# Kernel tuning notes

Measured on AMD Instinct MI355X. Metric: run time of the kernel, lower is better.

The kernel has to match this reference:

```python
import jax, jax.numpy as jnp
import numpy as np

G = 88        # voxel grid side
N = 200000    # active voxels
C = 64        # channels
P = 65536     # padded pairs per kernel offset
EPS = 1e-5


def _build_sparse_inputs():
    rng = np.random.default_rng(0)
    lin = rng.choice(G ** 3, size=N, replace=False)
    coords = np.stack(np.unravel_index(lin, (G, G, G)), axis=1).astype(np.int64)
    B = G + 2
    key = lambda c: ((c[:, 0] + 1) * B + (c[:, 1] + 1)) * B + (c[:, 2] + 1)
    keys = key(coords)
    order = np.argsort(keys)
    skeys = keys[order]
    offsets = [(i, j, k) for i in (-1, 0, 1) for j in (-1, 0, 1) for k in (-1, 0, 1)
               if (i, j, k) != (0, 0, 0)]
    in_maps = np.full((26, P), N, np.int32)   # sentinel N -> zero row
    out_maps = np.full((26, P), N, np.int32)  # sentinel N -> dump row
    for idx, off in enumerate(offsets):
        tgt = coords + np.array(off)
        tk = key(tgt)
        pos = np.clip(np.searchsorted(skeys, tk), 0, N - 1)
        valid = skeys[pos] == tk
        ii = order[pos[valid]]
        oo = np.nonzero(valid)[0]
        m = min(len(ii), P)
        in_maps[idx, :m] = ii[:m].astype(np.int32)
        out_maps[idx, :m] = oo[:m].astype(np.int32)
    return jnp.asarray(in_maps), jnp.asarray(out_maps)


def setup_inputs() -> dict:
    key = jax.random.key(0)
    ks = jax.random.split(key, 3)
    in_maps, out_maps = _build_sparse_inputs()
    return {
        "x": jax.random.normal(ks[0], (N, C), jnp.float32),
        "W1": jax.random.normal(ks[1], (27, C, C), jnp.float32) * 0.05,
        "gamma1": jnp.ones((C,), jnp.float32),
        "beta1": jnp.zeros((C,), jnp.float32),
        "W2": jax.random.normal(ks[2], (27, C, C), jnp.float32) * 0.05,
        "gamma2": jnp.ones((C,), jnp.float32),
        "beta2": jnp.zeros((C,), jnp.float32),
        "in_maps": in_maps,
        "out_maps": out_maps,
    }


def _sparse_conv3(feats, W, in_maps, out_maps):
    # feats: [N, Cin]; W: [27, Cin, Cout]; maps: [26, P] (center offset = W[13])
    n = feats.shape[0]
    zero_row = jnp.zeros((1, feats.shape[1]), feats.dtype)
    xp = jnp.concatenate([feats, zero_row], axis=0)          # [N+1, Cin]
    out = jnp.pad(feats @ W[13], ((0, 1), (0, 0)))            # center + dump row
    W_off = jnp.concatenate([W[:13], W[14:]], axis=0)         # [26, Cin, Cout]
    gathered = xp[in_maps]                                    # [26, P, Cin]
    contrib = jnp.einsum('kpc,kcd->kpd', gathered, W_off)     # [26, P, Cout]
    out = out.at[out_maps.reshape(-1)].add(contrib.reshape(-1, contrib.shape[-1]))
    return out[:n]


def _batch_norm(h, gamma, beta):
    mu = h.mean(axis=0)
    var = h.var(axis=0)  # biased, matches torch BN normalization
    return gamma * (h - mu) * jax.lax.rsqrt(var + EPS) + beta


def reference(x, W1, gamma1, beta1, W2, gamma2, beta2, in_maps, out_maps):
    out = _sparse_conv3(x, W1, in_maps, out_maps)
    out = jax.nn.relu(_batch_norm(out, gamma1, beta1))
    out = _batch_norm(_sparse_conv3(out, W2, in_maps, out_maps), gamma2, beta2)
    return jax.nn.relu(out + x)
```

## Files before the change

### kernel.cpp

```cpp
#include <hip/hip_runtime.h>
#include <hip/hip_bf16.h>


#define N_VOX 200000
#define NP 200192
#define EPS_BN 1e-5f

typedef __attribute__((ext_vector_type(8))) short bf16x8;
typedef __attribute__((ext_vector_type(4))) float f32x4;


__global__ void fill_kernel(int* __restrict__ nbrT, float* __restrict__ sums) {
    int p = blockIdx.y;
    long i = ((long)blockIdx.x * 256 + threadIdx.x) * 4;
    if (i < NP) {
        int4 v;
        if (p == 13) {
            v.x = (i + 0 < N_VOX) ? (int)i + 0 : N_VOX;
            v.y = (i + 1 < N_VOX) ? (int)i + 1 : N_VOX;
            v.z = (i + 2 < N_VOX) ? (int)i + 2 : N_VOX;
            v.w = (i + 3 < N_VOX) ? (int)i + 3 : N_VOX;
        } else {
            v.x = v.y = v.z = v.w = N_VOX;
        }
        *(int4*)(nbrT + (long)p * NP + i) = v;
    }
    if (p == 0 && blockIdx.x == 0 && threadIdx.x < 64) {
        float4 z = {0.f, 0.f, 0.f, 0.f};
        ((float4*)sums)[threadIdx.x] = z;
    }
}

__global__ void scatter_kernel(const int* __restrict__ out_maps,
                               const int* __restrict__ in_maps,
                               int* __restrict__ nbrT) {
    int idx = blockIdx.x * 256 + threadIdx.x;
    int o = out_maps[idx];
    if (o < N_VOX) {
        int k = idx >> 16;
        int p = k + (k >= 13);
        nbrT[(long)p * NP + o] = in_maps[idx];
    }
}

__global__ void cast_x_kernel(const float* __restrict__ x,
                              __hip_bfloat16* __restrict__ xb) {
    long i = ((long)blockIdx.x * 256 + threadIdx.x) * 4;
    if (i >= (long)(N_VOX + 1) * 64) return;
    __hip_bfloat16 t[4];
    if (i < (long)N_VOX * 64) {
        float4 v = *(const float4*)(x + i);
        t[0] = __float2bfloat16(v.x); t[1] = __float2bfloat16(v.y);
        t[2] = __float2bfloat16(v.z); t[3] = __float2bfloat16(v.w);
    } else {
        t[0] = t[1] = t[2] = t[3] = __float2bfloat16(0.0f);
    }
    *(ushort4*)(xb + i) = *(ushort4*)t;
}

__global__ void cast_w_kernel(const float* __restrict__ W1, const float* __restrict__ W2,
                              __hip_bfloat16* __restrict__ W1S, __hip_bfloat16* __restrict__ W2S) {
    int idx = blockIdx.x * 256 + threadIdx.x;
    if (idx >= 27 * 4096) return;
    int j    = idx & 7;
    int lane = (idx >> 3) & 63;
    int g    = idx >> 9;
    int half = g & 1, ct = (g >> 1) & 3, k = g >> 3;
    int m = lane & 15, quad = lane >> 4;
    int c = half * 32 + quad * 8 + j;
    int d = ct * 16 + m;
    int src = k * 4096 + c * 64 + d;
    W1S[idx] = __float2bfloat16(W1[src]);
    W2S[idx] = __float2bfloat16(W2[src]);
}


__global__ __launch_bounds__(256, 3) void conv_kernel(
    const __hip_bfloat16* __restrict__ xb,
    const __hip_bfloat16* __restrict__ W4,
    const int* __restrict__ nbrT,
    __hip_bfloat16* __restrict__ h,
    float* __restrict__ sums)
{
    const int tid  = threadIdx.x;
    const int lane = tid & 63;
    const int wave = tid >> 6;
    const int m    = lane & 15;
    const int quad = lane >> 4;
    const int blockbase = blockIdx.x * 256;
    const int rbase = blockbase + wave * 64;

    __shared__ __align__(16) char smem[52224];
    int*            sidx = (int*)smem;
    __hip_bfloat16* bbuf = (__hip_bfloat16*)(smem + 27648);
    float*          lsum = (float*)(smem + 44032);
    float*          lsq  = (float*)(smem + 48128);
    __hip_bfloat16* trans = (__hip_bfloat16*)(smem + wave * 9216);

    for (int j = tid; j < 27 * 256; j += 256)
        sidx[j] = nbrT[(long)(j >> 8) * NP + blockbase + (j & 255)];

    {
        const __hip_bfloat16* ws = W4 + wave * 1024 + lane * 8;
        bf16x8 b0 = *(const bf16x8*)(ws);
        bf16x8 b1 = *(const bf16x8*)(ws + 512);
        __hip_bfloat16* bd = bbuf + wave * 1024 + lane * 8;
        *(bf16x8*)bd = b0;
        *(bf16x8*)(bd + 512) = b1;
    }
    __syncthreads();

    f32x4 acc[16];
#pragma unroll
    for (int i = 0; i < 16; ++i) acc[i] = (f32x4){0.f, 0.f, 0.f, 0.f};

    const bf16x8 z8 = {0, 0, 0, 0, 0, 0, 0, 0};
    bf16x8 A[2][4][2];
    bf16x8 btr0, btr1;

#define LOAD_A(s, p)                                                        \
    {                                                                       \
        _Pragma("unroll")                                                   \
        for (int t = 0; t < 4; ++t) {                                       \
            int ii = sidx[(p) * 256 + wave * 64 + t * 16 + m];              \
            if (ii < N_VOX) {                                               \
                const __hip_bfloat16* rr = xb + (long)ii * 64 + quad * 8;   \
                A[s][t][0] = *(const bf16x8*)rr;                            \
                A[s][t][1] = *(const bf16x8*)(rr + 32);                     \
            } else { A[s][t][0] = z8; A[s][t][1] = z8; }                    \
        }                                                                   \
    }

#define LOAD_BT(p)                                                          \
    {                                                                       \
        const __hip_bfloat16* ws = W4 + (p) * 4096 + wave * 1024 + lane * 8;\
        btr0 = *(const bf16x8*)(ws);                                        \
        btr1 = *(const bf16x8*)(ws + 512);                                  \
    }

    LOAD_BT(1)
    LOAD_A(0, 0)

#pragma unroll
    for (int k = 0; k < 27; ++k) {
        asm volatile("s_waitcnt lgkmcnt(0)\n\ts_barrier" ::: "memory");
        if (k + 1 < 27) {
            __hip_bfloat16* bd = bbuf + ((k + 1) & 1) * 4096 + wave * 1024 + lane * 8;
            *(bf16x8*)bd = btr0;
            *(bf16x8*)(bd + 512) = btr1;
        }
        if (k + 2 < 27) LOAD_BT(k + 2)
        if (k + 1 < 27) LOAD_A((k + 1) & 1, k + 1)
        __builtin_amdgcn_sched_barrier(0);
        const __hip_bfloat16* bb = bbuf + (k & 1) * 4096;
        const int cs = k & 1;
#pragma unroll
        for (int ct = 0; ct < 4; ++ct) {
#pragma unroll
            for (int hf = 0; hf < 2; ++hf) {
                bf16x8 b = *(const bf16x8*)(bb + (ct * 2 + hf) * 512 + lane * 8);
#pragma unroll
                for (int t = 0; t < 4; ++t)
                    acc[t * 4 + ct] = __builtin_amdgcn_mfma_f32_16x16x32_bf16(A[cs][t][hf], b, acc[t * 4 + ct], 0, 0, 0);
            }
        }
        __builtin_amdgcn_sched_barrier(0);
    }
#undef LOAD_A
#undef LOAD_BT

    __syncthreads();

    const bool valid = rbase < N_VOX;

#pragma unroll
    for (int ct = 0; ct < 4; ++ct) {
        float s = 0.f, q = 0.f;
        if (valid) {
#pragma unroll
            for (int t = 0; t < 4; ++t)
#pragma unroll
                for (int r = 0; r < 4; ++r) {
                    float v = acc[t * 4 + ct][r];
                    s += v; q += v * v;
                }
        }
        lsum[(wave * 4 + quad) * 64 + ct * 16 + m] = s;
        lsq [(wave * 4 + quad) * 64 + ct * 16 + m] = q;
    }
    __syncthreads();
    if (tid < 64) {
        float S = 0.f, Q = 0.f;
#pragma unroll
        for (int j = 0; j < 16; ++j) { S += lsum[j * 64 + tid]; Q += lsq[j * 64 + tid]; }
        atomicAdd(&sums[tid], S);
        atomicAdd(&sums[64 + tid], Q);
    }

    if (valid) {
#pragma unroll
        for (int t = 0; t < 4; ++t)
#pragma unroll
            for (int r = 0; r < 4; ++r)
#pragma unroll
                for (int ct = 0; ct < 4; ++ct)
                    trans[(t * 16 + quad * 4 + r) * 72 + ct * 16 + m] =
                        __float2bfloat16(acc[t * 4 + ct][r]);
#pragma unroll
        for (int i = 0; i < 8; ++i) {
            int row = i * 8 + (lane >> 3);
            bf16x8 v = *(const bf16x8*)(trans + row * 72 + (lane & 7) * 8);
            *(bf16x8*)(h + (long)(rbase + row) * 64 + (lane & 7) * 8) = v;
        }
    }
}


__global__ void bnrelu_kernel(const __hip_bfloat16* __restrict__ h, const float* __restrict__ sums,
                              const float* __restrict__ gamma, const float* __restrict__ beta,
                              __hip_bfloat16* __restrict__ hb) {
    long i = ((long)blockIdx.x * 256 + threadIdx.x) * 4;
    if (i >= (long)(N_VOX + 1) * 64) return;
    __hip_bfloat16 t[4];
    if (i < (long)N_VOX * 64) {
        int c0 = (int)(i & 63);
        ushort4 raw = *(const ushort4*)(h + i);
        __hip_bfloat16 hv[4];
        *(ushort4*)hv = raw;
#pragma unroll
        for (int j = 0; j < 4; ++j) {
            int c = c0 + j;
            float mu  = sums[c] * (1.0f / N_VOX);
            float var = sums[64 + c] * (1.0f / N_VOX) - mu * mu;
            float rs  = rsqrtf(var + EPS_BN);
            float val = gamma[c] * (__bfloat162float(hv[j]) - mu) * rs + beta[c];
            t[j] = __float2bfloat16(fmaxf(val, 0.0f));
        }
    } else {
        t[0] = t[1] = t[2] = t[3] = __float2bfloat16(0.0f);
    }
    *(ushort4*)(hb + i) = *(ushort4*)t;
}


__global__ void final_kernel(const __hip_bfloat16* __restrict__ h, const float* __restrict__ x,
                             const float* __restrict__ sums, const float* __restrict__ gamma,
                             const float* __restrict__ beta, float* __restrict__ out) {
    long i = ((long)blockIdx.x * 256 + threadIdx.x) * 4;
    if (i >= (long)N_VOX * 64) return;
    int c0 = (int)(i & 63);
    ushort4 raw = *(const ushort4*)(h + i);
    __hip_bfloat16 hv[4];
    *(ushort4*)hv = raw;
    float4 xr = *(const float4*)(x + i);
    float xx[4] = {xr.x, xr.y, xr.z, xr.w};
    float oo[4];
#pragma unroll
    for (int j = 0; j < 4; ++j) {
        int c = c0 + j;
        float mu  = sums[c] * (1.0f / N_VOX);
        float var = sums[64 + c] * (1.0f / N_VOX) - mu * mu;
        float rs  = rsqrtf(var + EPS_BN);
        float val = gamma[c] * (__bfloat162float(hv[j]) - mu) * rs + beta[c] + xx[j];
        oo[j] = fmaxf(val, 0.0f);
    }
    float4 ov = {oo[0], oo[1], oo[2], oo[3]};
    *(float4*)(out + i) = ov;
}


extern "C" void kernel_launch(void* const* d_in, const int* in_sizes, int n_in,
                              void* d_out, int out_size, void* d_ws, size_t ws_size,
                              hipStream_t stream) {
    const float* x      = (const float*)d_in[0];
    const float* W1     = (const float*)d_in[1];
    const float* gamma1 = (const float*)d_in[2];
    const float* beta1  = (const float*)d_in[3];
    const float* W2     = (const float*)d_in[4];
    const float* gamma2 = (const float*)d_in[5];
    const float* beta2  = (const float*)d_in[6];
    const int* in_maps  = (const int*)d_in[7];
    const int* out_maps = (const int*)d_in[8];
    float* out = (float*)d_out;

    char* ws = (char*)d_ws;
    size_t off = 0;
    auto alloc = [&](size_t bytes) -> void* {
        void* p = ws + off;
        off = (off + bytes + 255) & ~(size_t)255;
        return p;
    };
    int* nbrT           = (int*)alloc((size_t)27 * NP * 4);
    __hip_bfloat16* xb  = (__hip_bfloat16*)alloc((size_t)(N_VOX + 1) * 64 * 2);
    __hip_bfloat16* W1S = (__hip_bfloat16*)alloc((size_t)27 * 4096 * 2);
    __hip_bfloat16* W2S = (__hip_bfloat16*)alloc((size_t)27 * 4096 * 2);
    __hip_bfloat16* h   = (__hip_bfloat16*)alloc((size_t)N_VOX * 64 * 2);
    float* sums         = (float*)alloc(256 * 4);
    __hip_bfloat16* h1b = xb;

    const long elem_x = (long)(N_VOX + 1) * 64;

    fill_kernel   <<<dim3((NP / 4 + 255) / 256, 27), 256, 0, stream>>>(nbrT, sums);
    scatter_kernel<<<26 * 65536 / 256, 256, 0, stream>>>(out_maps, in_maps, nbrT);
    cast_x_kernel <<<(int)((elem_x / 4 + 255) / 256), 256, 0, stream>>>(x, xb);
    cast_w_kernel <<<(27 * 4096 + 255) / 256, 256, 0, stream>>>(W1, W2, W1S, W2S);

    conv_kernel   <<<NP / 256, 256, 0, stream>>>(xb, W1S, nbrT, h, sums);
    bnrelu_kernel <<<(int)((elem_x / 4 + 255) / 256), 256, 0, stream>>>(h, sums, gamma1, beta1, h1b);

    conv_kernel   <<<NP / 256, 256, 0, stream>>>(h1b, W2S, nbrT, h, sums + 128);
    final_kernel  <<<(int)(((long)N_VOX * 64 / 4 + 255) / 256), 256, 0, stream>>>(h, x, sums + 128, gamma2, beta2, out);
}
```

Baseline: 340.5 us.

## Vectorize neighbor index loads, reduce BN stats via wave shuffles, template sentinel check

The 27x256 neighbor-index tile is now loaded as int4 vectors instead of scalar ints. Per-block BN statistics are reduced with cross-quad wave shuffles and direct per-wave atomics, which removes the LDS lsum/lsq buffers and one barrier and cuts shared memory so more blocks may fit. A DIAG template parameter drops the sentinel branch for the first conv. That relies on xb holding a zeroed extra row at index N_VOX, while the second conv keeps the check. Atomic traffic to the sums array rises fourfold in exchange.

```diff
diff --git a/kernel.cpp b/kernel.cpp
--- a/kernel.cpp
+++ b/kernel.cpp
@@ -75,6 +75,7 @@
 }
 
 
+template<int DIAG>
 __global__ __launch_bounds__(256, 3) void conv_kernel(
     const __hip_bfloat16* __restrict__ xb,
     const __hip_bfloat16* __restrict__ W4,
@@ -90,15 +91,15 @@
     const int blockbase = blockIdx.x * 256;
     const int rbase = blockbase + wave * 64;
 
-    __shared__ __align__(16) char smem[52224];
+    __shared__ __align__(16) char smem[44032];
     int*            sidx = (int*)smem;
     __hip_bfloat16* bbuf = (__hip_bfloat16*)(smem + 27648);
-    float*          lsum = (float*)(smem + 44032);
-    float*          lsq  = (float*)(smem + 48128);
     __hip_bfloat16* trans = (__hip_bfloat16*)(smem + wave * 9216);
 
-    for (int j = tid; j < 27 * 256; j += 256)
-        sidx[j] = nbrT[(long)(j >> 8) * NP + blockbase + (j & 255)];
+    for (int j = tid; j < 1728; j += 256) {
+        int p = j >> 6, w = j & 63;
+        ((int4*)sidx)[j] = *(const int4*)(nbrT + (long)p * NP + blockbase + w * 4);
+    }
 
     {
         const __hip_bfloat16* ws = W4 + wave * 1024 + lane * 8;
@@ -123,7 +124,11 @@
         _Pragma("unroll")                                                   \
         for (int t = 0; t < 4; ++t) {                                       \
             int ii = sidx[(p) * 256 + wave * 64 + t * 16 + m];              \
-            if (ii < N_VOX) {                                               \
+            if (DIAG) {    \
+                const __hip_bfloat16* rr = xb + (long)ii * 64 + quad * 8;   \
+                A[s][t][0] = *(const bf16x8*)rr;                            \
+                A[s][t][1] = *(const bf16x8*)(rr + 32);                     \
+            } else if (ii < N_VOX) {                                        \
                 const __hip_bfloat16* rr = xb + (long)ii * 64 + quad * 8;   \
                 A[s][t][0] = *(const bf16x8*)rr;                            \
                 A[s][t][1] = *(const bf16x8*)(rr + 32);                     \
@@ -169,14 +174,12 @@
 #undef LOAD_A
 #undef LOAD_BT
 
-    __syncthreads();
-
     const bool valid = rbase < N_VOX;
 
-#pragma unroll
-    for (int ct = 0; ct < 4; ++ct) {
-        float s = 0.f, q = 0.f;
-        if (valid) {
+    if (valid) {
+#pragma unroll
+        for (int ct = 0; ct < 4; ++ct) {
+            float s = 0.f, q = 0.f;
 #pragma unroll
             for (int t = 0; t < 4; ++t)
 #pragma unroll
@@ -184,18 +187,16 @@
                     float v = acc[t * 4 + ct][r];
                     s += v; q += v * v;
                 }
-        }
-        lsum[(wave * 4 + quad) * 64 + ct * 16 + m] = s;
-        lsq [(wave * 4 + quad) * 64 + ct * 16 + m] = q;
-    }
+            s += __shfl_xor(s, 16); s += __shfl_xor(s, 32);
+            q += __shfl_xor(q, 16); q += __shfl_xor(q, 32);
+            if (quad == 0) {
+                atomicAdd(&sums[ct * 16 + m], s);
+                atomicAdd(&sums[64 + ct * 16 + m], q);
+            }
+        }
+    }
+
     __syncthreads();
-    if (tid < 64) {
-        float S = 0.f, Q = 0.f;
-#pragma unroll
-        for (int j = 0; j < 16; ++j) { S += lsum[j * 64 + tid]; Q += lsq[j * 64 + tid]; }
-        atomicAdd(&sums[tid], S);
-        atomicAdd(&sums[64 + tid], Q);
-    }
 
     if (valid) {
 #pragma unroll
@@ -305,9 +306,9 @@
     cast_x_kernel <<<(int)((elem_x / 4 + 255) / 256), 256, 0, stream>>>(x, xb);
     cast_w_kernel <<<(27 * 4096 + 255) / 256, 256, 0, stream>>>(W1, W2, W1S, W2S);
 
-    conv_kernel   <<<NP / 256, 256, 0, stream>>>(xb, W1S, nbrT, h, sums);
+    conv_kernel<1><<<NP / 256, 256, 0, stream>>>(xb, W1S, nbrT, h, sums);
     bnrelu_kernel <<<(int)((elem_x / 4 + 255) / 256), 256, 0, stream>>>(h, sums, gamma1, beta1, h1b);
 
-    conv_kernel   <<<NP / 256, 256, 0, stream>>>(h1b, W2S, nbrT, h, sums + 128);
+    conv_kernel<0><<<NP / 256, 256, 0, stream>>>(h1b, W2S, nbrT, h, sums + 128);
     final_kernel  <<<(int)(((long)N_VOX * 64 / 4 + 255) / 256), 256, 0, stream>>>(h, x, sums + 128, gamma2, beta2, out);
 }
```

Result: slower. 429.2 us (+26.0%).
